# Performance work log

Measured on AMD Instinct MI355X. Metric: run time of the kernel, lower is better.

The kernel has to match this reference:

```python
import jax, jax.numpy as jnp
import numpy as np

_CNOT = np.array([[1,0,0,0],[0,1,0,0],[0,0,0,1],[0,0,1,0]], dtype=np.complex64)


def _ry(t):
    c = jnp.cos(0.5 * t).astype(jnp.complex64)
    s = jnp.sin(0.5 * t).astype(jnp.complex64)
    return jnp.stack([jnp.stack([c, -s]), jnp.stack([s, c])])


def _rx(t):
    c = jnp.cos(0.5 * t).astype(jnp.complex64)
    s = (-1j * jnp.sin(0.5 * t)).astype(jnp.complex64)
    return jnp.stack([jnp.stack([c, s]), jnp.stack([s, c])])


def _rz(t):
    z = jnp.zeros((), jnp.complex64)
    em = jnp.exp(-0.5j * t).astype(jnp.complex64)
    ep = jnp.exp(0.5j * t).astype(jnp.complex64)
    return jnp.stack([jnp.stack([em, z]), jnp.stack([z, ep])])


def _apply_1q(state, gate, wire):
    # state: [B, P, 2, 2, 2, 2]; wire axis is 2 + wire
    state = jnp.moveaxis(state, 2 + wire, -1)
    state = jnp.einsum('ij,...j->...i', gate, state)
    return jnp.moveaxis(state, -1, 2 + wire)


def _apply_2q(state, gate, w1, w2):
    state = jnp.moveaxis(state, (2 + w1, 2 + w2), (-2, -1))
    sh = state.shape
    state = state.reshape(sh[:-2] + (4,))
    state = jnp.einsum('ij,...j->...i', gate, state)
    return jnp.moveaxis(state.reshape(sh), (-2, -1), (2 + w1, 2 + w2))


def _forward(x, theta, W, b):
    B = x.shape[0]
    # non-overlapping 2x2 patches, order [x[r,c], x[r,c+1], x[r+1,c], x[r+1,c+1]]
    p = x.reshape(B, 14, 2, 14, 2).transpose(0, 1, 3, 2, 4).reshape(B, 196, 4)
    half = 0.5 * p
    amp = jnp.stack([jnp.cos(half), jnp.sin(half)], axis=-1).astype(jnp.complex64)  # [B,196,4,2]
    # RY encoding from |0000> gives a product state over the 4 wires
    state = jnp.einsum('bpi,bpj,bpk,bpl->bpijkl', amp[:, :, 0], amp[:, :, 1], amp[:, :, 2], amp[:, :, 3])
    cnot = jnp.asarray(_CNOT)
    # fixed 8-op "random layer" (RandomLayer(n_ops=8) realization, 6 trainable angles)
    state = _apply_1q(state, _rx(theta[0]), 0)
    state = _apply_1q(state, _ry(theta[1]), 1)
    state = _apply_1q(state, _rz(theta[2]), 2)
    state = _apply_1q(state, _rx(theta[3]), 3)
    state = _apply_2q(state, cnot, 0, 1)
    state = _apply_2q(state, cnot, 2, 3)
    state = _apply_1q(state, _ry(theta[4]), 0)
    state = _apply_1q(state, _rz(theta[5]), 3)
    probs = state.real ** 2 + state.imag ** 2  # [B,196,2,2,2,2]
    z = jnp.array([1.0, -1.0], jnp.float32)
    e0 = jnp.einsum('bpijkl,i->bp', probs, z)
    e1 = jnp.einsum('bpijkl,j->bp', probs, z)
    e2 = jnp.einsum('bpijkl,k->bp', probs, z)
    e3 = jnp.einsum('bpijkl,l->bp', probs, z)
    feats = jnp.stack([e0, e1, e2, e3], axis=-1).reshape(B, 4 * 14 * 14)
    logits = feats @ W.T + b
    return jax.nn.log_softmax(logits, axis=-1)


def setup_inputs() -> dict:
    key = jax.random.key(0)
    k1, k2, k3 = jax.random.split(key, 3)
    B = 4096
    x = jax.random.uniform(k1, (B, 28, 28), dtype=jnp.float32) * np.float32(np.pi)
    theta = jax.random.uniform(k2, (6,), dtype=jnp.float32) * np.float32(2 * np.pi)
    W = jax.random.normal(k3, (10, 784), dtype=jnp.float32) * 0.02
    b = jnp.zeros((10,), jnp.float32)
    return {"x": x, "theta": theta, "W": W, "b": b}


def reference(x, theta, W, b):
    return _forward(x, theta, W, b)
```

## Files before the change

kernel.cpp:

```cpp
#include <hip/hip_runtime.h>
#include <math.h>

__global__ __launch_bounds__(256) void quanv_fused_kernel(
    const float* __restrict__ x,
    const float* __restrict__ theta,
    const float* __restrict__ W,
    const float* __restrict__ bias,
    float* __restrict__ out,
    int B)
{
    const int wave = threadIdx.x >> 6;
    const int lane = threadIdx.x & 63;
    const int b    = blockIdx.x * 4 + wave;
    if (b >= B) return;

    float sx0, cx0, sy1, cy1, sy4, cy4;
    __sincosf(0.5f * theta[0], &sx0, &cx0);
    __sincosf(0.5f * theta[1], &sy1, &cy1);
    __sincosf(0.5f * theta[4], &sy4, &cy4);
    const float cth3 = __cosf(theta[3]);

    const float* __restrict__ xb = x + (size_t)b * 784;

    float acc[10];
#pragma unroll
    for (int k = 0; k < 10; ++k) acc[k] = 0.f;

    for (int p = lane; p < 196; p += 64) {
        const int r = p / 14, c = p - r * 14;
        const float* px = xb + r * 56 + c * 2;
        const float p0 = px[0];
        const float p1 = px[1];
        const float p2 = px[28];
        const float p3 = px[29];

        float s0, c0, s1, c1;
        __sincosf(0.5f * p0, &s0, &c0);
        __sincosf(0.5f * p1, &s1, &c1);
        const float cp2 = __cosf(p2);
        const float cp3 = __cosf(p3);

        const float v0 = c0 * c1, v1 = c0 * s1, v2 = s0 * c1, v3 = s0 * s1;
        const float Ar0 =  cx0 * v0, Ai0 = -sx0 * v2;
        const float Ar1 =  cx0 * v1, Ai1 = -sx0 * v3;
        const float Ar2 =  cx0 * v2, Ai2 = -sx0 * v0;
        const float Ar3 =  cx0 * v3, Ai3 = -sx0 * v1;
        const float Br0 = cy1 * Ar0 - sy1 * Ar1, Bi0 = cy1 * Ai0 - sy1 * Ai1;
        const float Br1 = sy1 * Ar0 + cy1 * Ar1, Bi1 = sy1 * Ai0 + cy1 * Ai1;
        const float Br2 = cy1 * Ar2 - sy1 * Ar3, Bi2 = cy1 * Ai2 - sy1 * Ai3;
        const float Br3 = sy1 * Ar2 + cy1 * Ar3, Bi3 = sy1 * Ai2 + cy1 * Ai3;
        const float Cr2 = Br3, Ci2 = Bi3;
        const float Cr3 = Br2, Ci3 = Bi2;
        const float Dr0 = cy4 * Br0 - sy4 * Cr2, Di0 = cy4 * Bi0 - sy4 * Ci2;
        const float Dr2 = sy4 * Br0 + cy4 * Cr2, Di2 = sy4 * Bi0 + cy4 * Ci2;
        const float Dr1 = cy4 * Br1 - sy4 * Cr3, Di1 = cy4 * Bi1 - sy4 * Ci3;
        const float Dr3 = sy4 * Br1 + cy4 * Cr3, Di3 = sy4 * Bi1 + cy4 * Ci3;

        const float q0 = Dr0 * Dr0 + Di0 * Di0;
        const float q1 = Dr1 * Dr1 + Di1 * Di1;
        const float q2 = Dr2 * Dr2 + Di2 * Di2;
        const float q3 = Dr3 * Dr3 + Di3 * Di3;
        const float e0 = q0 + q1 - q2 - q3;
        const float e1 = q0 - q1 + q2 - q3;
        const float e2 = cp2;
        const float e3 = cth3 * cp2 * cp3;

#pragma unroll
        for (int k = 0; k < 10; ++k) {
            const float4 w4 = *reinterpret_cast<const float4*>(&W[k * 784 + 4 * p]);
            acc[k] += e0 * w4.x + e1 * w4.y + e2 * w4.z + e3 * w4.w;
        }
    }

#pragma unroll
    for (int m = 1; m < 64; m <<= 1) {
#pragma unroll
        for (int k = 0; k < 10; ++k) acc[k] += __shfl_xor(acc[k], m, 64);
    }

    if (lane == 0) {
        float logit[10];
        float mx = -1e30f;
#pragma unroll
        for (int k = 0; k < 10; ++k) {
            const float v = acc[k] + bias[k];
            logit[k] = v;
            mx = fmaxf(mx, v);
        }
        float s = 0.f;
#pragma unroll
        for (int k = 0; k < 10; ++k) s += __expf(logit[k] - mx);
        const float lse = mx + __logf(s);
#pragma unroll
        for (int k = 0; k < 10; ++k) out[(size_t)b * 10 + k] = logit[k] - lse;
    }
}

extern "C" void kernel_launch(void* const* d_in, const int* in_sizes, int n_in,
                              void* d_out, int out_size, void* d_ws, size_t ws_size,
                              hipStream_t stream) {
    const float* x     = (const float*)d_in[0];
    const float* theta = (const float*)d_in[1];
    const float* W     = (const float*)d_in[2];
    const float* bias  = (const float*)d_in[3];
    float* out = (float*)d_out;

    const int B = in_sizes[0] / 784;
    const int blocks = (B + 3) / 4;
    quanv_fused_kernel<<<dim3(blocks), dim3(256), 0, stream>>>(x, theta, W, bias, out, B);
}
```

Baseline: 13.93 us.

## Collapse circuit into closed-form expectation values and parallelize softmax epilogue

Replaces the per-patch complex statevector gate simulation with closed-form trig expressions for the four Pauli-Z expectations, folding theta into precomputed constants and one shifted sincos. It also loads pixel pairs as float2, fully unrolls the patch loop into three full iterations plus a tail, and spreads the log-softmax across ten lanes using shuffles instead of doing it serially on lane 0. This removes most per-patch ALU work, but the closed form must match the reference exactly, and the fast intrinsics are applied to larger arguments than before.

```diff
diff --git a/kernel.cpp b/kernel.cpp
--- a/kernel.cpp
+++ b/kernel.cpp
@@ -14,11 +14,11 @@
     const int b    = blockIdx.x * 4 + wave;
     if (b >= B) return;
 
-    float sx0, cx0, sy1, cy1, sy4, cy4;
-    __sincosf(0.5f * theta[0], &sx0, &cx0);
-    __sincosf(0.5f * theta[1], &sy1, &cy1);
-    __sincosf(0.5f * theta[4], &sy4, &cy4);
-    const float cth3 = __cosf(theta[3]);
+    const float t1 = theta[1];
+    const float K1 = __cosf(theta[0]) * __cosf(theta[4]);
+    const float K2 = __sinf(theta[4]);
+    const float K3 = __cosf(theta[0]);
+    const float K4 = __cosf(theta[3]);
 
     const float* __restrict__ xb = x + (size_t)b * 784;
 
@@ -26,51 +26,33 @@
 #pragma unroll
     for (int k = 0; k < 10; ++k) acc[k] = 0.f;
 
-    for (int p = lane; p < 196; p += 64) {
+    auto do_patch = [&](int p) {
         const int r = p / 14, c = p - r * 14;
         const float* px = xb + r * 56 + c * 2;
-        const float p0 = px[0];
-        const float p1 = px[1];
-        const float p2 = px[28];
-        const float p3 = px[29];
+        const float2 t01 = *reinterpret_cast<const float2*>(px);
+        const float2 t23 = *reinterpret_cast<const float2*>(px + 28);
 
-        float s0, c0, s1, c1;
-        __sincosf(0.5f * p0, &s0, &c0);
-        __sincosf(0.5f * p1, &s1, &c1);
-        const float cp2 = __cosf(p2);
-        const float cp3 = __cosf(p3);
+        float sp0, cp0, sph, cph;
+        __sincosf(t01.x, &sp0, &cp0);
+        __sincosf(t01.y + t1, &sph, &cph);
+        const float cp2 = __cosf(t23.x);
+        const float cp3 = __cosf(t23.y);
 
-        const float v0 = c0 * c1, v1 = c0 * s1, v2 = s0 * c1, v3 = s0 * s1;
-        const float Ar0 =  cx0 * v0, Ai0 = -sx0 * v2;
-        const float Ar1 =  cx0 * v1, Ai1 = -sx0 * v3;
-        const float Ar2 =  cx0 * v2, Ai2 = -sx0 * v0;
-        const float Ar3 =  cx0 * v3, Ai3 = -sx0 * v1;
-        const float Br0 = cy1 * Ar0 - sy1 * Ar1, Bi0 = cy1 * Ai0 - sy1 * Ai1;
-        const float Br1 = sy1 * Ar0 + cy1 * Ar1, Bi1 = sy1 * Ai0 + cy1 * Ai1;
-        const float Br2 = cy1 * Ar2 - sy1 * Ar3, Bi2 = cy1 * Ai2 - sy1 * Ai3;
-        const float Br3 = sy1 * Ar2 + cy1 * Ar3, Bi3 = sy1 * Ai2 + cy1 * Ai3;
-        const float Cr2 = Br3, Ci2 = Bi3;
-        const float Cr3 = Br2, Ci3 = Bi2;
-        const float Dr0 = cy4 * Br0 - sy4 * Cr2, Di0 = cy4 * Bi0 - sy4 * Ci2;
-        const float Dr2 = sy4 * Br0 + cy4 * Cr2, Di2 = sy4 * Bi0 + cy4 * Ci2;
-        const float Dr1 = cy4 * Br1 - sy4 * Cr3, Di1 = cy4 * Bi1 - sy4 * Ci3;
-        const float Dr3 = sy4 * Br1 + cy4 * Cr3, Di3 = sy4 * Bi1 + cy4 * Ci3;
-
-        const float q0 = Dr0 * Dr0 + Di0 * Di0;
-        const float q1 = Dr1 * Dr1 + Di1 * Di1;
-        const float q2 = Dr2 * Dr2 + Di2 * Di2;
-        const float q3 = Dr3 * Dr3 + Di3 * Di3;
-        const float e0 = q0 + q1 - q2 - q3;
-        const float e1 = q0 - q1 + q2 - q3;
+        const float e0 = K1 * cp0 - K2 * sp0 * sph;
+        const float e1 = K3 * cp0 * cph;
         const float e2 = cp2;
-        const float e3 = cth3 * cp2 * cp3;
+        const float e3 = K4 * cp2 * cp3;
 
 #pragma unroll
         for (int k = 0; k < 10; ++k) {
             const float4 w4 = *reinterpret_cast<const float4*>(&W[k * 784 + 4 * p]);
             acc[k] += e0 * w4.x + e1 * w4.y + e2 * w4.z + e3 * w4.w;
         }
-    }
+    };
+
+#pragma unroll
+    for (int i = 0; i < 3; ++i) do_patch(lane + 64 * i);
+    if (lane < 4) do_patch(192 + lane);
 
 #pragma unroll
     for (int m = 1; m < 64; m <<= 1) {
@@ -78,22 +60,20 @@
         for (int k = 0; k < 10; ++k) acc[k] += __shfl_xor(acc[k], m, 64);
     }
 
-    if (lane == 0) {
-        float logit[10];
-        float mx = -1e30f;
+    float v = acc[0];
 #pragma unroll
-        for (int k = 0; k < 10; ++k) {
-            const float v = acc[k] + bias[k];
-            logit[k] = v;
-            mx = fmaxf(mx, v);
-        }
-        float s = 0.f;
+    for (int k = 1; k < 10; ++k) v = (lane == k) ? acc[k] : v;
+    v += bias[lane < 10 ? lane : 0];
+
+    float m = (lane < 10) ? v : -1e30f;
 #pragma unroll
-        for (int k = 0; k < 10; ++k) s += __expf(logit[k] - mx);
-        const float lse = mx + __logf(s);
+    for (int off = 1; off < 16; off <<= 1) m = fmaxf(m, __shfl_xor(m, off, 16));
+    float s = (lane < 10) ? __expf(v - m) : 0.f;
 #pragma unroll
-        for (int k = 0; k < 10; ++k) out[(size_t)b * 10 + k] = logit[k] - lse;
-    }
+    for (int off = 1; off < 16; off <<= 1) s += __shfl_xor(s, off, 16);
+    const float lse = m + __logf(s);
+
+    if (lane < 10) out[(size_t)b * 10 + lane] = v - lse;
 }
 
 extern "C" void kernel_launch(void* const* d_in, const int* in_sizes, int n_in,
```

Result: faster. 13.27 us (-4.7%).
